# Performance work log

Measured on AMD Instinct MI355X. Metric: run time of the kernel, lower is better.

## Reference

```python
import jax, jax.numpy as jnp
import numpy as np

COUNTS = [1536, 8192, 16384, 24576, 12288, 1024, 512, 512, 256, 128, 128]
OFFS = np.concatenate([[0], np.cumsum(COUNTS)]).astype(int).tolist()
N = OFFS[-1]          # 65536 atoms total, sorted by degree
MAX_DEG = 10
BATCH = 2048          # fixed GraphGather batch size
F_IN = 75
GC = 256
DENSE = 512
N_TASKS = 12
N_CLASSES = 2
BN_EPS = 1e-3         # keras BatchNormalization default epsilon


def _graph_conv(x, deg_adjs, w0, wself, wneigh, b):
    # deepchem GraphConv: per-degree (self @ Wself + sum_neighbors @ Wneigh + b), relu
    outs = [x[OFFS[0]:OFFS[1]] @ w0 + b[0]]  # degree-0 atoms: self transform only
    for d in range(1, MAX_DEG + 1):
        self_atoms = x[OFFS[d]:OFFS[d + 1]]            # [n_d, F]
        neigh = x[deg_adjs[d - 1]].sum(axis=1)         # gather [n_d, d, F] -> sum -> [n_d, F]
        outs.append(self_atoms @ wself[d - 1] + neigh @ wneigh[d - 1] + b[d])
    return jax.nn.relu(jnp.concatenate(outs, axis=0))


def _graph_pool(x, deg_adjs):
    # deepchem GraphPool: elementwise max over {self} U neighbors, per degree
    outs = [x[OFFS[0]:OFFS[1]]]  # degree-0 atoms pass through
    for d in range(1, MAX_DEG + 1):
        self_atoms = x[OFFS[d]:OFFS[d + 1]]
        outs.append(jnp.maximum(self_atoms, x[deg_adjs[d - 1]].max(axis=1)))
    return jnp.concatenate(outs, axis=0)


def _bn(x, g, bta, m, v):
    # inference-mode BatchNormalization (training=False -> moving stats)
    return g * (x - m) * jax.lax.rsqrt(v + BN_EPS) + bta


def setup_inputs():
    key = jax.random.key(0)
    ks = iter(jax.random.split(key, 64))
    inp = {}
    inp["atom_features"] = jax.random.normal(next(ks), (N, F_IN), jnp.float32)
    inp["degree_slice"] = jnp.asarray(
        np.stack([np.array(OFFS[:-1]), np.array(COUNTS)], axis=1), jnp.int32)
    # each molecule gets exactly N/BATCH atoms so no GraphGather segment is empty
    inp["membership"] = jax.random.permutation(
        next(ks), jnp.arange(N, dtype=jnp.int32) % BATCH)
    inp["n_samples"] = BATCH
    for d in range(1, MAX_DEG + 1):
        inp["deg_adj_%d" % d] = jax.random.randint(
            next(ks), (COUNTS[d], d), 0, N, jnp.int32)

    def lin(k, fi, fo):
        return jax.random.normal(k, (fi, fo), jnp.float32) * np.float32(1.0 / np.sqrt(fi))

    for li, fi in [(1, F_IN), (2, GC)]:
        inp["gc%d_w0" % li] = lin(next(ks), fi, GC)
        inp["gc%d_wself" % li] = jnp.stack([lin(next(ks), fi, GC) for _ in range(MAX_DEG)])
        inp["gc%d_wneigh" % li] = jnp.stack([lin(next(ks), fi, GC) for _ in range(MAX_DEG)])
        inp["gc%d_b" % li] = jnp.zeros((MAX_DEG + 1, GC), jnp.float32)
    for bi, dim in [(1, GC), (2, GC), (3, DENSE)]:
        inp["bn%d_gamma" % bi] = jnp.ones((dim,), jnp.float32)
        inp["bn%d_beta" % bi] = jnp.zeros((dim,), jnp.float32)
        inp["bn%d_mean" % bi] = jnp.zeros((dim,), jnp.float32)
        inp["bn%d_var" % bi] = jnp.ones((dim,), jnp.float32)
    inp["dense_w"] = lin(next(ks), GC, DENSE)
    inp["dense_b"] = jnp.zeros((DENSE,), jnp.float32)
    inp["out_w"] = lin(next(ks), 2 * DENSE, N_TASKS * N_CLASSES)
    inp["out_b"] = jnp.zeros((N_TASKS * N_CLASSES,), jnp.float32)
    return inp


def reference(atom_features, degree_slice, membership, n_samples,
              deg_adj_1, deg_adj_2, deg_adj_3, deg_adj_4, deg_adj_5,
              deg_adj_6, deg_adj_7, deg_adj_8, deg_adj_9, deg_adj_10,
              gc1_w0, gc1_wself, gc1_wneigh, gc1_b,
              gc2_w0, gc2_wself, gc2_wneigh, gc2_b,
              bn1_gamma, bn1_beta, bn1_mean, bn1_var,
              bn2_gamma, bn2_beta, bn2_mean, bn2_var,
              bn3_gamma, bn3_beta, bn3_mean, bn3_var,
              dense_w, dense_b, out_w, out_b):
    deg_adjs = [deg_adj_1, deg_adj_2, deg_adj_3, deg_adj_4, deg_adj_5,
                deg_adj_6, deg_adj_7, deg_adj_8, deg_adj_9, deg_adj_10]
    h = _graph_conv(atom_features, deg_adjs, gc1_w0, gc1_wself, gc1_wneigh, gc1_b)
    h = _bn(h, bn1_gamma, bn1_beta, bn1_mean, bn1_var)
    h = _graph_pool(h, deg_adjs)
    h = _graph_conv(h, deg_adjs, gc2_w0, gc2_wself, gc2_wneigh, gc2_b)
    h = _bn(h, bn2_gamma, bn2_beta, bn2_mean, bn2_var)
    h = _graph_pool(h, deg_adjs)
    h = jax.nn.relu(h @ dense_w + dense_b)
    h = _bn(h, bn3_gamma, bn3_beta, bn3_mean, bn3_var)
    # GraphGather: tanh(concat(segment_sum, segment_max))
    ssum = jax.ops.segment_sum(h, membership, num_segments=BATCH)
    smax = jax.ops.segment_max(h, membership, num_segments=BATCH)
    fp = jnp.tanh(jnp.concatenate([ssum, smax], axis=1))   # [BATCH, 2*DENSE]
    logits = (fp @ out_w + out_b).reshape(BATCH, N_TASKS, N_CLASSES)[:n_samples]
    probs = jax.nn.softmax(logits, axis=-1)
    return probs, logits, fp
```

## Files before the change

### kernel.cpp

```cpp
#include <hip/hip_runtime.h>
#include <hip/hip_fp16.h>
#include <math.h>

#define NATOMS 65536

typedef _Float16 f16_t;
typedef __attribute__((ext_vector_type(8))) _Float16 half8;
typedef __attribute__((ext_vector_type(4))) float f32x4;

__constant__ int c_offs[12] = {0,1536,9728,26112,50688,62976,64000,64512,65024,65280,65408,65536};

struct Adj { const int* p[10]; };

__device__ __forceinline__ int seg_of(int row) {
    int s = 0;
#pragma unroll
    for (int i = 1; i <= 10; ++i) s += (row >= c_offs[i]) ? 1 : 0;
    return s;
}

__device__ __forceinline__ void glds16(const f16_t* g, f16_t* l) {
    __builtin_amdgcn_global_load_lds(
        (const __attribute__((address_space(1))) unsigned int*)g,
        (__attribute__((address_space(3))) unsigned int*)l,
        16, 0, 0);
}

__device__ __forceinline__ half8 max8(half8 a, half8 b) {
    half8 r;
#pragma unroll
    for (int e = 0; e < 8; ++e) r[e] = (a[e] >= b[e]) ? a[e] : b[e];
    return r;
}


__global__ void pack_cvt(const float* __restrict__ g1w0, const float* __restrict__ g1ws,
                         const float* __restrict__ g1wn,
                         const float* __restrict__ g2w0, const float* __restrict__ g2ws,
                         const float* __restrict__ g2wn,
                         const float* __restrict__ dw, const float* __restrict__ ow,
                         f16_t* __restrict__ W1p, f16_t* __restrict__ W2p,
                         f16_t* __restrict__ Wdp, f16_t* __restrict__ Wop,
                         int* __restrict__ counts,
                         const float* __restrict__ xf, f16_t* __restrict__ xq) {
    if (blockIdx.x >= 8384) {
        int idx = (blockIdx.x - 8384) * 256 + threadIdx.x;
        int r = idx / 12;
        int cc = idx - r * 12;
        int c = cc << 3;
        f16_t o[8];
#pragma unroll
        for (int e = 0; e < 8; ++e)
            o[e] = (c + e < 75) ? (f16_t)xf[(size_t)r*75 + c + e] : (f16_t)0.f;
        *(uint4*)(xq + (size_t)r*96 + c) = *(uint4*)o;
        return;
    }
    int idx = blockIdx.x * 256 + threadIdx.x;
    if (idx < 2048) counts[idx] = 0;
    if (idx < 540672) {
        int j = idx & 7, lane = (idx >> 3) & 63;
        int kb = (idx >> 9) % 6;
        int rest = idx / (512 * 6);
        int ni = rest & 15, s = rest >> 4;
        int k = kb * 32 + (lane >> 4) * 8 + j;
        int n = ni * 16 + (lane & 15);
        float v = 0.f;
        if (k < 75) v = (s == 0) ? g1w0[k*256 + n] : g1ws[((s-1)*75 + k)*256 + n];
        else if (k >= 96 && k < 171 && s > 0) v = g1wn[((s-1)*75 + (k-96))*256 + n];
        W1p[idx] = (f16_t)v;
    } else if (idx < 1982464) {
        int i2 = idx - 540672;
        int j = i2 & 7, lane = (i2 >> 3) & 63;
        int kb = (i2 >> 9) & 15;
        int rest = i2 >> 13;
        int ni = rest & 15, s = rest >> 4;
        int k = kb * 32 + (lane >> 4) * 8 + j;
        int n = ni * 16 + (lane & 15);
        float v = 0.f;
        if (k < 256) v = (s == 0) ? g2w0[k*256 + n] : g2ws[((s-1)*256 + k)*256 + n];
        else if (s > 0) v = g2wn[((s-1)*256 + (k-256))*256 + n];
        W2p[i2] = (f16_t)v;
    } else if (idx < 2113536) {
        int i2 = idx - 1982464;
        int j = i2 & 7, lane = (i2 >> 3) & 63;
        int kb = (i2 >> 9) & 7;
        int ni = (i2 >> 12) & 31;
        int k = kb * 32 + (lane >> 4) * 8 + j;
        int n = ni * 16 + (lane & 15);
        Wdp[i2] = (f16_t)dw[(size_t)k*512 + n];
    } else {
        int i2 = idx - 2113536;
        int j = i2 & 7, lane = (i2 >> 3) & 63;
        int kb = (i2 >> 9) & 31;
        int ni = i2 >> 14;
        int k = kb * 32 + (lane >> 4) * 8 + j;
        int n = ni * 16 + (lane & 15);
        Wop[i2] = (n < 24) ? (f16_t)ow[k*24 + n] : (f16_t)0.f;
    }
}

template<int D, int LD>
__device__ __forceinline__ void gathD(float* v, const f16_t* __restrict__ src,
                                      const int* __restrict__ ap, int c) {
    int rows[D];
#pragma unroll
    for (int j = 0; j < D; ++j) rows[j] = ap[j];
    uint4 raw[D];
#pragma unroll
    for (int j = 0; j < D; ++j) raw[j] = *(const uint4*)(src + (size_t)rows[j]*LD + c);
#pragma unroll
    for (int j = 0; j < D; ++j) {
        const f16_t* u = (const f16_t*)&raw[j];
#pragma unroll
        for (int e = 0; e < 8; ++e) v[e] += (float)u[e];
    }
}

template<int LD>
__device__ __forceinline__ void gath_sum(float* v, const f16_t* __restrict__ src,
                                         const int* __restrict__ ap, int s, int c) {
    switch (s) {
        case 1:  gathD<1,LD>(v,src,ap,c);  break;
        case 2:  gathD<2,LD>(v,src,ap,c);  break;
        case 3:  gathD<3,LD>(v,src,ap,c);  break;
        case 4:  gathD<4,LD>(v,src,ap,c);  break;
        case 5:  gathD<5,LD>(v,src,ap,c);  break;
        case 6:  gathD<6,LD>(v,src,ap,c);  break;
        case 7:  gathD<7,LD>(v,src,ap,c);  break;
        case 8:  gathD<8,LD>(v,src,ap,c);  break;
        case 9:  gathD<9,LD>(v,src,ap,c);  break;
        case 10: gathD<10,LD>(v,src,ap,c); break;
        default: break;
    }
}

template<int D, int LD>
__device__ __forceinline__ void gathD_pk(half8& v, const f16_t* __restrict__ src,
                                         const int* __restrict__ ap, int c) {
    int rows[D];
#pragma unroll
    for (int j = 0; j < D; ++j) rows[j] = ap[j];
    half8 raw[D];
#pragma unroll
    for (int j = 0; j < D; ++j) raw[j] = *(const half8*)(src + (size_t)rows[j]*LD + c);
#pragma unroll
    for (int j = 0; j < D; ++j) v = max8(v, raw[j]);
}

template<int LD>
__device__ __forceinline__ void gath_max(half8& v, const f16_t* __restrict__ src,
                                         const int* __restrict__ ap, int s, int c) {
    switch (s) {
        case 1:  gathD_pk<1,LD>(v,src,ap,c);  break;
        case 2:  gathD_pk<2,LD>(v,src,ap,c);  break;
        case 3:  gathD_pk<3,LD>(v,src,ap,c);  break;
        case 4:  gathD_pk<4,LD>(v,src,ap,c);  break;
        case 5:  gathD_pk<5,LD>(v,src,ap,c);  break;
        case 6:  gathD_pk<6,LD>(v,src,ap,c);  break;
        case 7:  gathD_pk<7,LD>(v,src,ap,c);  break;
        case 8:  gathD_pk<8,LD>(v,src,ap,c);  break;
        case 9:  gathD_pk<9,LD>(v,src,ap,c);  break;
        case 10: gathD_pk<10,LD>(v,src,ap,c); break;
        default: break;
    }
}

__global__ __launch_bounds__(256) void nbsum_sc(const f16_t* __restrict__ xq,
                                                f16_t* __restrict__ NBX, Adj adj,
                                                const int* __restrict__ mem,
                                                int* __restrict__ counts,
                                                int* __restrict__ slots) {
    if (blockIdx.x >= 3072) {
        int i = (blockIdx.x - 3072) * 256 + threadIdx.x;
        int s = mem[i];
        int p = atomicAdd(&counts[s], 1);
        if (p < 32) slots[s*32 + p] = i;
        return;
    }
    int idx = blockIdx.x * 256 + threadIdx.x;
    int r = (int)((unsigned)idx / 12u);
    int cc = idx - r * 12;
    int c = cc << 3;
    int s = seg_of(r);
    float v[8];
#pragma unroll
    for (int e = 0; e < 8; ++e) v[e] = 0.f;
    if (s > 0)
        gath_sum<96>(v, xq, adj.p[s-1] + (size_t)(r - c_offs[s]) * s, s, c);
    f16_t o[8];
#pragma unroll
    for (int e = 0; e < 8; ++e) o[e] = (f16_t)v[e];
    *(uint4*)(NBX + (size_t)(r>>4)*1536 + (c>>5)*512 + ((c>>3)&3)*128 + (r&15)*8) = *(uint4*)o;
}

template<bool BLOB>
__global__ __launch_bounds__(256) void pool_k(const f16_t* __restrict__ H,
                                              f16_t* __restrict__ P, Adj adj) {
    int idx = blockIdx.x * 256 + threadIdx.x;
    int r = idx >> 5;
    int c = (idx & 31) << 3;
    int s = seg_of(r);
    half8 v = *(const half8*)(H + (size_t)r*256 + c);
    if (s > 0)
        gath_max<256>(v, H, adj.p[s-1] + (size_t)(r - c_offs[s]) * s, s, c);
    if (BLOB)
        *(half8*)(P + (size_t)(r>>4)*4096 + (c>>5)*512 + ((c>>3)&3)*128 + (r&15)*8) = v;
    else
        *(half8*)(P + (size_t)r*256 + c) = v;
}

__global__ __launch_bounds__(256) void nbsum_k(const f16_t* __restrict__ P,
                                               f16_t* __restrict__ NB, Adj adj) {
    int idx = blockIdx.x * 256 + threadIdx.x;
    int r = idx >> 5;
    int c = (idx & 31) << 3;
    int s = seg_of(r);
    float v[8];
#pragma unroll
    for (int e = 0; e < 8; ++e) v[e] = 0.f;
    if (s > 0)
        gath_sum<256>(v, P, adj.p[s-1] + (size_t)(r - c_offs[s]) * s, s, c);
    f16_t o[8];
#pragma unroll
    for (int e = 0; e < 8; ++e) o[e] = (f16_t)v[e];
    *(uint4*)(NB + (size_t)(r>>4)*4096 + (c>>5)*512 + ((c>>3)&3)*128 + (r&15)*8) = *(uint4*)o;
}

template<int NKB, int KSPB, int LDA, int NKBA1, int NY, int N, bool SEG>
__global__ __launch_bounds__(512, 2)
void gemm256(const f16_t* __restrict__ A0, const f16_t* __restrict__ A1,
             const f16_t* __restrict__ Wp,
             const float* __restrict__ bias,
             const float* __restrict__ bng, const float* __restrict__ bnb,
             const float* __restrict__ bnm, const float* __restrict__ bnv,
             f16_t* __restrict__ C)
{
    constexpr int NT  = NKB / 2;
    constexpr int NNT = N / 16;
    __shared__ f16_t sm[65536];

    const int t = threadIdx.x;
    const int lane = t & 63, w = t >> 6;
    const int wm = w >> 2, wn = w & 3;
    const int quad = lane >> 4, l16 = lane & 15;
    const int id = blockIdx.x;
    const int xi = id / NY, y = id - xi * NY;
    const int r0 = xi * 256;
    const int n0 = y * 256;
    const int rtg = r0 >> 4;
    const int nbase = n0 >> 4;
    const int segB = SEG ? seg_of(r0) : 0;
    const bool strad = SEG && (seg_of(r0 + 255) != segB);
    const int segw = SEG ? seg_of(r0 + wm*128) : 0;

    f32x4 acc[8][4];
#pragma unroll
    for (int mi = 0; mi < 8; ++mi)
#pragma unroll
        for (int ni = 0; ni < 4; ++ni) acc[mi][ni] = (f32x4){0.f,0.f,0.f,0.f};

    size_t aoff[2];
#pragma unroll
    for (int i = 0; i < 2; ++i)
        aoff[i] = (size_t)(r0 + (w*2 + i)*16 + l16) * LDA + quad*8;

    auto stage = [&](int kt, int buf) {
        f16_t* bb = sm + buf*32768;
#pragma unroll
        for (int i = 0; i < 2; ++i) {
            const int rt = w*2 + i;
#pragma unroll
            for (int kb2 = 0; kb2 < 2; ++kb2) {
                const int kb = kt*2 + kb2;
                if constexpr (KSPB > 0) {
                    if (kb < KSPB)
                        glds16(A0 + (size_t)kb*32 + aoff[i], bb + (rt*2 + kb2)*512);
                    else
                        glds16(A1 + ((size_t)(rtg + rt)*NKBA1 + (kb - KSPB))*512 + lane*8,
                               bb + (rt*2 + kb2)*512);
                } else {
                    glds16(A1 + ((size_t)(rtg + rt)*NKBA1 + kb)*512 + lane*8,
                           bb + (rt*2 + kb2)*512);
                }
                glds16(Wp + ((size_t)(segB*NNT + nbase + rt)*NKB + kb)*512 + lane*8,
                       bb + 16384 + (rt*2 + kb2)*512);
            }
        }
    };

    stage(0, 0);
    __syncthreads();

    for (int kt = 0; kt < NT; ++kt) {
        const int buf = kt & 1;
        if (kt + 1 < NT) stage(kt + 1, buf ^ 1);
        const f16_t* bb = sm + buf*32768;

        half8 bfr[4][2];
        if (strad) {
#pragma unroll
            for (int ni = 0; ni < 4; ++ni)
#pragma unroll
                for (int kb2 = 0; kb2 < 2; ++kb2)
                    bfr[ni][kb2] = *(const half8*)(Wp +
                        ((size_t)(segw*NNT + nbase + wn*4 + ni)*NKB + kt*2 + kb2)*512 + lane*8);
        } else {
#pragma unroll
            for (int ni = 0; ni < 4; ++ni)
#pragma unroll
                for (int kb2 = 0; kb2 < 2; ++kb2)
                    bfr[ni][kb2] = *(const half8*)(bb + 16384 +
                        ((wn*4 + ni)*2 + kb2)*512 + lane*8);
        }

#pragma unroll
        for (int ph = 0; ph < 4; ++ph) {
            half8 a[2][2];
#pragma unroll
            for (int m2 = 0; m2 < 2; ++m2)
#pragma unroll
                for (int kb2 = 0; kb2 < 2; ++kb2)
                    a[m2][kb2] = *(const half8*)(bb +
                        ((wm*8 + ph*2 + m2)*2 + kb2)*512 + lane*8);
#pragma unroll
            for (int m2 = 0; m2 < 2; ++m2)
#pragma unroll
                for (int ni = 0; ni < 4; ++ni)
#pragma unroll
                    for (int kb2 = 0; kb2 < 2; ++kb2)
                        acc[ph*2 + m2][ni] = __builtin_amdgcn_mfma_f32_16x16x32_f16(
                            a[m2][kb2], bfr[ni][kb2], acc[ph*2 + m2][ni], 0, 0, 0);
        }
        __syncthreads();
    }

    f16_t* eps = sm;
#pragma unroll
    for (int s = 0; s < 4; ++s) {
        if (wm == (s >> 1)) {
#pragma unroll
            for (int ni = 0; ni < 4; ++ni) {
                const int lcol = wn*64 + ni*16 + l16;
                const int col = n0 + lcol;
                const float scale = bng[col] * rsqrtf(bnv[col] + 1e-3f);
                const float shift = bnb[col] - bnm[col] * scale;
                const float bv = bias[(SEG ? segw*N : 0) + col];
#pragma unroll
                for (int m2 = 0; m2 < 4; ++m2) {
                    const int mi = (s & 1)*4 + m2;
                    const int rowb = m2*16 + quad*4;
#pragma unroll
                    for (int rr = 0; rr < 4; ++rr) {
                        float v = acc[mi][ni][rr] + bv;
                        v = fmaxf(v, 0.f);
                        v = fmaf(v, scale, shift);
                        eps[(rowb + rr)*264 + lcol] = (f16_t)v;
                    }
                }
            }
        }
        __syncthreads();
#pragma unroll
        for (int k = 0; k < 4; ++k) {
            int idx = k*512 + t;
            int row = idx >> 5, ch = idx & 31;
            *(uint4*)(C + (size_t)(r0 + s*64 + row)*N + n0 + ch*8) =
                *(const uint4*)&eps[row*264 + ch*8];
        }
        __syncthreads();
    }
}

__global__ __launch_bounds__(256)
void reduce_k(const f16_t* __restrict__ H3, const int* __restrict__ slots,
              float* __restrict__ fp) {
    __shared__ float shs[3][512];
    __shared__ float shm[3][512];
    int s = blockIdx.x;
    int t = threadIdx.x;
    int w = t >> 6, l = t & 63;
    int c = l * 8;
    const int* sl = slots + s*32 + w*8;
    float sm[8], mx[8];
#pragma unroll
    for (int e = 0; e < 8; ++e) { sm[e] = 0.f; mx[e] = -INFINITY; }
#pragma unroll
    for (int i = 0; i < 8; ++i) {
        int a = sl[i];
        uint4 raw = *(const uint4*)(H3 + (size_t)a*512 + c);
        const f16_t* u = (const f16_t*)&raw;
#pragma unroll
        for (int e = 0; e < 8; ++e) {
            float f = (float)u[e];
            sm[e] += f;
            mx[e] = fmaxf(mx[e], f);
        }
    }
    if (w) {
        *(float4*)&shs[w-1][c]   = *(float4*)&sm[0];
        *(float4*)&shs[w-1][c+4] = *(float4*)&sm[4];
        *(float4*)&shm[w-1][c]   = *(float4*)&mx[0];
        *(float4*)&shm[w-1][c+4] = *(float4*)&mx[4];
    }
    __syncthreads();
    if (w == 0) {
#pragma unroll
        for (int j = 0; j < 3; ++j)
#pragma unroll
            for (int e = 0; e < 8; ++e) {
                sm[e] += shs[j][c+e];
                mx[e] = fmaxf(mx[e], shm[j][c+e]);
            }
        float o1[8], o2[8];
#pragma unroll
        for (int e = 0; e < 8; ++e) {
            o1[e] = tanhf(sm[e]); o2[e] = tanhf(mx[e]);
        }
        float* fr = fp + (size_t)s*1024;
        *(float4*)(fr + c)       = *(float4*)&o1[0];
        *(float4*)(fr + c + 4)   = *(float4*)&o1[4];
        *(float4*)(fr + 512 + c)     = *(float4*)&o2[0];
        *(float4*)(fr + 512 + c + 4) = *(float4*)&o2[4];
    }
}

__global__ __launch_bounds__(64)
void final_mfma(const float* __restrict__ fp, const f16_t* __restrict__ Wop,
                const float* __restrict__ out_b,
                float* __restrict__ probs, float* __restrict__ logits) {
    const int t = threadIdx.x;
    const int lane = t & 63;
    const int quad = lane >> 4, l16 = lane & 15;
    const int r0 = blockIdx.x * 16;

    f32x4 acc[2];
#pragma unroll
    for (int ni = 0; ni < 2; ++ni) acc[ni] = (f32x4){0.f,0.f,0.f,0.f};

    const size_t rowoff = (size_t)(r0 + l16) * 1024 + quad*8;
    size_t boff[2];
#pragma unroll
    for (int ni = 0; ni < 2; ++ni)
        boff[ni] = (size_t)ni * 32 * 512 + lane*8;

    auto loadA = [&](half8& a, int kb) {
        const float* src = fp + rowoff + kb*32;
        float4 u0 = *(const float4*)(src);
        float4 u1 = *(const float4*)(src + 4);
        half8 h;
        h[0] = (f16_t)u0.x; h[1] = (f16_t)u0.y; h[2] = (f16_t)u0.z; h[3] = (f16_t)u0.w;
        h[4] = (f16_t)u1.x; h[5] = (f16_t)u1.y; h[6] = (f16_t)u1.z; h[7] = (f16_t)u1.w;
        a = h;
    };
    auto loadB = [&](half8* b, int kb) {
#pragma unroll
        for (int ni = 0; ni < 2; ++ni) b[ni] = *(const half8*)(Wop + boff[ni] + (size_t)kb*512);
    };
    auto domfma = [&](half8& a, half8* b) {
#pragma unroll
        for (int ni = 0; ni < 2; ++ni)
            acc[ni] = __builtin_amdgcn_mfma_f32_16x16x32_f16(a, b[ni], acc[ni], 0, 0, 0);
    };

    half8 a0, b0[2], a1, b1[2];
    loadA(a0, 0); loadB(b0, 0);
#pragma unroll
    for (int kb = 0; kb < 32; kb += 2) {
        loadA(a1, kb + 1); loadB(b1, kb + 1);
        domfma(a0, b0);
        if (kb + 2 < 32) { loadA(a0, kb + 2); loadB(b0, kb + 2); }
        domfma(a1, b1);
    }

#pragma unroll
    for (int ni = 0; ni < 2; ++ni) {
        const int c = ni*16 + l16;
        const bool ok = (c < 24);
        const float bv = ok ? out_b[c] : 0.f;
#pragma unroll
        for (int r = 0; r < 4; ++r) {
            float lg = acc[ni][r] + bv;
            float lp = __shfl_xor(lg, 1);
            float m = fmaxf(lg, lp);
            float e  = expf(lg - m);
            float ep = expf(lp - m);
            float pr = e / (e + ep);
            if (ok) {
                int row = r0 + quad*4 + r;
                logits[(size_t)row*24 + c] = lg;
                probs[(size_t)row*24 + c]  = pr;
            }
        }
    }
}

extern "C" void kernel_launch(void* const* d_in, const int* in_sizes, int n_in,
                              void* d_out, int out_size, void* d_ws, size_t ws_size,
                              hipStream_t stream) {
    const float* atom       = (const float*)d_in[0];
    const int*   membership = (const int*)  d_in[2];
    Adj adj;
    for (int d = 0; d < 10; ++d) adj.p[d] = (const int*)d_in[4+d];
    const float* gc1_w0     = (const float*)d_in[14];
    const float* gc1_wself  = (const float*)d_in[15];
    const float* gc1_wneigh = (const float*)d_in[16];
    const float* gc1_b      = (const float*)d_in[17];
    const float* gc2_w0     = (const float*)d_in[18];
    const float* gc2_wself  = (const float*)d_in[19];
    const float* gc2_wneigh = (const float*)d_in[20];
    const float* gc2_b      = (const float*)d_in[21];
    const float* bn1g = (const float*)d_in[22]; const float* bn1b = (const float*)d_in[23];
    const float* bn1m = (const float*)d_in[24]; const float* bn1v = (const float*)d_in[25];
    const float* bn2g = (const float*)d_in[26]; const float* bn2b = (const float*)d_in[27];
    const float* bn2m = (const float*)d_in[28]; const float* bn2v = (const float*)d_in[29];
    const float* bn3g = (const float*)d_in[30]; const float* bn3b = (const float*)d_in[31];
    const float* bn3m = (const float*)d_in[32]; const float* bn3v = (const float*)d_in[33];
    const float* dense_w = (const float*)d_in[34];
    const float* dense_b = (const float*)d_in[35];
    const float* out_w   = (const float*)d_in[36];
    const float* out_b   = (const float*)d_in[37];

    f16_t* wsb = (f16_t*)d_ws;
    f16_t* xq    = wsb;
    f16_t* NBX   = wsb + 6291456;
    f16_t* H1b   = wsb + 12582912;
    f16_t* P1rm  = wsb + 29360128;
    f16_t* NB2b  = wsb + 46137344;
    f16_t* H2b   = H1b;
    f16_t* P2bl  = NB2b;
    f16_t* H3b   = H1b;
    f16_t* W1p   = wsb + 62914560;
    f16_t* W2p   = wsb + 63455232;
    f16_t* Wdp   = wsb + 64897024;
    f16_t* Wop   = wsb + 65028096;
    int*  counts = (int*)(wsb + 65060864);
    int*  slots  = counts + 2048;

    float* outp   = (float*)d_out;
    float* probs  = outp;
    float* logits = outp + 49152;
    float* fp     = outp + 98304;

    pack_cvt<<<11456, 256, 0, stream>>>(gc1_w0, gc1_wself, gc1_wneigh,
                                        gc2_w0, gc2_wself, gc2_wneigh,
                                        dense_w, out_w,
                                        W1p, W2p, Wdp, Wop, counts,
                                        atom, xq);

    nbsum_sc<<<3328, 256, 0, stream>>>(xq, NBX, adj, membership, counts, slots);
    gemm256<6,3,96,3,1,256,true><<<256, 512, 0, stream>>>(
        xq, NBX, W1p, gc1_b, bn1g, bn1b, bn1m, bn1v, H1b);
    pool_k<false><<<(NATOMS*32)/256, 256, 0, stream>>>(H1b, P1rm, adj);

    nbsum_k<<<(NATOMS*32)/256, 256, 0, stream>>>(P1rm, NB2b, adj);
    gemm256<16,8,256,8,1,256,true><<<256, 512, 0, stream>>>(
        P1rm, NB2b, W2p, gc2_b, bn2g, bn2b, bn2m, bn2v, H2b);
    pool_k<true><<<(NATOMS*32)/256, 256, 0, stream>>>(H2b, P2bl, adj);

    gemm256<8,0,1,8,2,512,false><<<512, 512, 0, stream>>>(
        P2bl, P2bl, Wdp, dense_b, bn3g, bn3b, bn3m, bn3v, H3b);

    reduce_k<<<2048, 256, 0, stream>>>(H3b, slots, fp);

    final_mfma<<<128, 64, 0, stream>>>(fp, Wop, out_b, probs, logits);
}
```

Before: 340.3 us.

## Switch GEMM staging to triple-buffered single-K-block pipeline with vmcnt waits

The GEMM main loop now stages one 32-wide K block per step into a three-slot LDS ring instead of two K blocks into a double buffer. It waits with explicit s_waitcnt vmcnt plus a single barrier per step, so two loads can be in flight while the current slot is computed. LDS use drops from 128KB to 96KB, but there are twice as many iterations and barriers. The vmcnt(4) count is hand-tuned to the number of async loads each stage issues, which makes it fragile if that count changes.

```diff
diff --git a/kernel.cpp b/kernel.cpp
--- a/kernel.cpp
+++ b/kernel.cpp
@@ -235,9 +235,9 @@
              const float* __restrict__ bnm, const float* __restrict__ bnv,
              f16_t* __restrict__ C)
 {
-    constexpr int NT  = NKB / 2;
+    constexpr int NT  = NKB;
     constexpr int NNT = N / 16;
-    __shared__ f16_t sm[65536];
+    __shared__ f16_t sm[49152];
 
     const int t = threadIdx.x;
     const int lane = t & 63, w = t >> 6;
@@ -264,75 +264,64 @@
     for (int i = 0; i < 2; ++i)
         aoff[i] = (size_t)(r0 + (w*2 + i)*16 + l16) * LDA + quad*8;
 
-    auto stage = [&](int kt, int buf) {
-        f16_t* bb = sm + buf*32768;
+    auto stage = [&](int kb, int buf) {
+        f16_t* bb = sm + buf*16384;
 #pragma unroll
         for (int i = 0; i < 2; ++i) {
             const int rt = w*2 + i;
-#pragma unroll
-            for (int kb2 = 0; kb2 < 2; ++kb2) {
-                const int kb = kt*2 + kb2;
-                if constexpr (KSPB > 0) {
-                    if (kb < KSPB)
-                        glds16(A0 + (size_t)kb*32 + aoff[i], bb + (rt*2 + kb2)*512);
-                    else
-                        glds16(A1 + ((size_t)(rtg + rt)*NKBA1 + (kb - KSPB))*512 + lane*8,
-                               bb + (rt*2 + kb2)*512);
-                } else {
-                    glds16(A1 + ((size_t)(rtg + rt)*NKBA1 + kb)*512 + lane*8,
-                           bb + (rt*2 + kb2)*512);
-                }
-                glds16(Wp + ((size_t)(segB*NNT + nbase + rt)*NKB + kb)*512 + lane*8,
-                       bb + 16384 + (rt*2 + kb2)*512);
+            if constexpr (KSPB > 0) {
+                if (kb < KSPB)
+                    glds16(A0 + (size_t)kb*32 + aoff[i], bb + rt*512);
+                else
+                    glds16(A1 + ((size_t)(rtg + rt)*NKBA1 + (kb - KSPB))*512 + lane*8,
+                           bb + rt*512);
+            } else {
+                glds16(A1 + ((size_t)(rtg + rt)*NKBA1 + kb)*512 + lane*8,
+                       bb + rt*512);
             }
+            glds16(Wp + ((size_t)(segB*NNT + nbase + rt)*NKB + kb)*512 + lane*8,
+                   bb + 8192 + rt*512);
         }
     };
 
     stage(0, 0);
+    stage(1, 1);
+
+    for (int kt = 0; kt < NT; ++kt) {
+        if (kt + 1 < NT) asm volatile("s_waitcnt vmcnt(4)" ::: "memory");
+        else             asm volatile("s_waitcnt vmcnt(0)" ::: "memory");
+        __builtin_amdgcn_s_barrier();
+        if (kt + 2 < NT) stage(kt + 2, (kt + 2) % 3);
+
+        const f16_t* bb = sm + (kt % 3)*16384;
+
+        half8 bfr[4];
+        if (strad) {
+#pragma unroll
+            for (int ni = 0; ni < 4; ++ni)
+                bfr[ni] = *(const half8*)(Wp +
+                    ((size_t)(segw*NNT + nbase + wn*4 + ni)*NKB + kt)*512 + lane*8);
+        } else {
+#pragma unroll
+            for (int ni = 0; ni < 4; ++ni)
+                bfr[ni] = *(const half8*)(bb + 8192 + (wn*4 + ni)*512 + lane*8);
+        }
+
+#pragma unroll
+        for (int ph = 0; ph < 4; ++ph) {
+            half8 a[2];
+#pragma unroll
+            for (int m2 = 0; m2 < 2; ++m2)
+                a[m2] = *(const half8*)(bb + (wm*8 + ph*2 + m2)*512 + lane*8);
+#pragma unroll
+            for (int m2 = 0; m2 < 2; ++m2)
+#pragma unroll
+                for (int ni = 0; ni < 4; ++ni)
+                    acc[ph*2 + m2][ni] = __builtin_amdgcn_mfma_f32_16x16x32_f16(
+                        a[m2], bfr[ni], acc[ph*2 + m2][ni], 0, 0, 0);
+        }
+    }
     __syncthreads();
-
-    for (int kt = 0; kt < NT; ++kt) {
-        const int buf = kt & 1;
-        if (kt + 1 < NT) stage(kt + 1, buf ^ 1);
-        const f16_t* bb = sm + buf*32768;
-
-        half8 bfr[4][2];
-        if (strad) {
-#pragma unroll
-            for (int ni = 0; ni < 4; ++ni)
-#pragma unroll
-                for (int kb2 = 0; kb2 < 2; ++kb2)
-                    bfr[ni][kb2] = *(const half8*)(Wp +
-                        ((size_t)(segw*NNT + nbase + wn*4 + ni)*NKB + kt*2 + kb2)*512 + lane*8);
-        } else {
-#pragma unroll
-            for (int ni = 0; ni < 4; ++ni)
-#pragma unroll
-                for (int kb2 = 0; kb2 < 2; ++kb2)
-                    bfr[ni][kb2] = *(const half8*)(bb + 16384 +
-                        ((wn*4 + ni)*2 + kb2)*512 + lane*8);
-        }
-
-#pragma unroll
-        for (int ph = 0; ph < 4; ++ph) {
-            half8 a[2][2];
-#pragma unroll
-            for (int m2 = 0; m2 < 2; ++m2)
-#pragma unroll
-                for (int kb2 = 0; kb2 < 2; ++kb2)
-                    a[m2][kb2] = *(const half8*)(bb +
-                        ((wm*8 + ph*2 + m2)*2 + kb2)*512 + lane*8);
-#pragma unroll
-            for (int m2 = 0; m2 < 2; ++m2)
-#pragma unroll
-                for (int ni = 0; ni < 4; ++ni)
-#pragma unroll
-                    for (int kb2 = 0; kb2 < 2; ++kb2)
-                        acc[ph*2 + m2][ni] = __builtin_amdgcn_mfma_f32_16x16x32_f16(
-                            a[m2][kb2], bfr[ni][kb2], acc[ph*2 + m2][ni], 0, 0, 0);
-        }
-        __syncthreads();
-    }
 
     f16_t* eps = sm;
 #pragma unroll
```

After: 389.5 us. 14.5% more time.
